# Optimization experiments

Measured on AMD Instinct MI355X. Metric: run time of the kernel, lower is better.

## Reference

```python
import jax, jax.numpy as jnp
import numpy as np

N = 50000   # nodes
E = 800000  # edges (avg degree 16)
D = 64      # node/edge feature dim
L = 3       # num_layers


def setup_inputs() -> dict:
    key = jax.random.key(0)
    ks = jax.random.split(key, 16)
    s = 0.05
    inp = {
        "x": jax.random.normal(ks[0], (N, D), jnp.float32),
        "edge_index": jax.random.randint(ks[1], (2, E), 0, N),
        "edge_attr": jax.random.normal(ks[2], (E, D), jnp.float32),
        # conv params (stacked over layers)
        "Wr": jax.random.normal(ks[3], (L, D, D), jnp.float32) * s,
        "Wn": jax.random.normal(ks[4], (L, D, D), jnp.float32) * s,
        "We": jax.random.normal(ks[5], (L, D, D), jnp.float32) * s,
        "b":  jax.random.normal(ks[6], (L, D), jnp.float32) * s,
        # EdgeMLP params (stacked over layers; only first L-1 used)
        "EWe": jax.random.normal(ks[7], (L, D, D), jnp.float32) * s,
        "Ebe": jax.random.normal(ks[8], (L, D), jnp.float32) * s,
        "EWs": jax.random.normal(ks[9], (L, D, D), jnp.float32) * s,
        "Ebs": jax.random.normal(ks[10], (L, D), jnp.float32) * s,
        "EWt": jax.random.normal(ks[11], (L, D, D), jnp.float32) * s,
        "Ebt": jax.random.normal(ks[12], (L, D), jnp.float32) * s,
        "EW1": jax.random.normal(ks[13], (L, D, D), jnp.float32) * s,
        "Eb1": jax.random.normal(ks[14], (L, D), jnp.float32) * s,
    }
    return inp


def reference(x, edge_index, edge_attr, Wr, Wn, We, b,
              EWe, Ebe, EWs, Ebs, EWt, Ebt, EW1, Eb1):
    src, dst = edge_index[0], edge_index[1]
    # in-degree for mean aggregation (static across layers)
    deg = jax.ops.segment_sum(jnp.ones((E,), x.dtype), dst, num_segments=N)
    inv_deg = (1.0 / jnp.clip(deg, 1.0))[:, None]  # [N,1]

    for i in range(L):
        # conv: message = x_src @ Wn + edge_attr @ We ; mean-aggregate at dst
        msg = x[src] @ Wn[i] + edge_attr @ We[i]              # [E,D]
        agg = jax.ops.segment_sum(msg, dst, num_segments=N) * inv_deg
        x = x @ Wr[i] + agg + b[i]                            # [N,D]
        if i == L - 1:
            break  # no act/norm/dropout/edge-update after last conv
        x = jax.nn.relu(x)  # act (norm=None, act_first=False, dropout p=0)
        # EdgeMLP: lin_e(ea) + lin_s(x)[src] + lin_t(x)[dst] -> act -> lin1
        h = (edge_attr @ EWe[i] + Ebe[i]
             + (x @ EWs[i] + Ebs[i])[src]
             + (x @ EWt[i] + Ebt[i])[dst])                    # [E,D]
        edge_attr = jax.nn.relu(h) @ EW1[i] + Eb1[i]
    return (x, edge_attr)
```

## Files before the change

### kernel.cpp

```cpp
#include <hip/hip_runtime.h>

#define D 64
#define LAYERS 3

typedef float  f4  __attribute__((ext_vector_type(4)));
typedef short  s8v __attribute__((ext_vector_type(8)));
typedef short  s4v __attribute__((ext_vector_type(4)));
typedef unsigned short ushort_t;

__device__ __forceinline__ unsigned short f2bf(float x) {
    unsigned int u = __float_as_uint(x);
    unsigned int r = (u + 0x7fffu + ((u >> 16) & 1u)) >> 16;
    return (unsigned short)r;
}
__device__ __forceinline__ float bf2f(unsigned short h) {
    return __uint_as_float(((unsigned int)h) << 16);
}


__global__ void k_count(const int* __restrict__ dst, int* __restrict__ cnt, int E) {
    int e = blockIdx.x * blockDim.x + threadIdx.x;
    if (e < E) atomicAdd(&cnt[dst[e]], 1);
}

__global__ __launch_bounds__(1024) void k_scan(const int* __restrict__ cnt,
                                               int* __restrict__ row_start,
                                               float* __restrict__ inv_deg, int N) {
    __shared__ int buf[1024];
    int tid = threadIdx.x;
    int per = (N + 1023) >> 10;
    int begin = tid * per;
    int end = min(begin + per, N);
    int s = 0;
    for (int i = begin; i < end; i++) s += cnt[i];
    buf[tid] = s;
    __syncthreads();
    for (int off = 1; off < 1024; off <<= 1) {
        int v = 0;
        if (tid >= off) v = buf[tid - off];
        __syncthreads();
        buf[tid] += v;
        __syncthreads();
    }
    int run = buf[tid] - s;
    for (int i = begin; i < end; i++) {
        row_start[i] = run;
        int c = cnt[i];
        inv_deg[i] = 1.0f / (float)(c > 1 ? c : 1);
        run += c;
    }
    if (begin < N && end == N) row_start[N] = run;
}

__global__ void k_fill(const int* __restrict__ src, const int* __restrict__ dst,
                       const int* __restrict__ row_start, int* __restrict__ cursor,
                       int* __restrict__ eids, int* __restrict__ srcs,
                       int* __restrict__ pdst, int* __restrict__ pos, int E) {
    int e = blockIdx.x * blockDim.x + threadIdx.x;
    if (e >= E) return;
    int d = dst[e];
    int p = row_start[d] + atomicAdd(&cursor[d], 1);
    eids[p] = e;
    srcs[p] = src[e];
    pdst[p] = d;
    pos[e] = p;
}

__global__ __launch_bounds__(256) void k_permcvt(const float* __restrict__ ea,
                                                 const int* __restrict__ pos,
                                                 ushort_t* __restrict__ pea, int E,
                                                 const float* __restrict__ x,
                                                 ushort_t* __restrict__ xb, int xtotal8,
                                                 int pblocks) {
    if ((int)blockIdx.x < pblocks) {
        int t = blockIdx.x * blockDim.x + threadIdx.x;
        int e = t >> 3;
        if (e >= E) return;
        int seg = t & 7;
        const float* rp = ea + (size_t)e * D + seg * 8;
        f4 a0 = *(const f4*)rp;
        f4 a1 = *(const f4*)(rp + 4);
        s8v o;
        #pragma unroll
        for (int i = 0; i < 4; i++) {
            o[i]     = (short)f2bf(a0[i]);
            o[4 + i] = (short)f2bf(a1[i]);
        }
        int p = pos[e];
        *(s8v*)(pea + (size_t)p * D + seg * 8) = o;
    } else {
        int t = (blockIdx.x - pblocks) * blockDim.x + threadIdx.x;
        if (t >= xtotal8) return;
        const float* rp = x + (size_t)t * 8;
        f4 a0 = *(const f4*)rp;
        f4 a1 = *(const f4*)(rp + 4);
        s8v o;
        #pragma unroll
        for (int i = 0; i < 4; i++) {
            o[i]     = (short)f2bf(a0[i]);
            o[4 + i] = (short)f2bf(a1[i]);
        }
        *(s8v*)(xb + (size_t)t * 8) = o;
    }
}

__global__ __launch_bounds__(64) void k_prepw(const float* __restrict__ Wr,
                                              const float* __restrict__ Wn,
                                              const float* __restrict__ Wec,
                                              const float* __restrict__ EWe,
                                              const float* __restrict__ EW1,
                                              const float* __restrict__ EWs,
                                              const float* __restrict__ EWt,
                                              s8v* __restrict__ wbuf) {
    int set = blockIdx.x;
    const float* Wsrc;
    int order, part;
    if (set < 18) {
        int i = set / 6, r = set % 6, m = r >> 1;
        part = r & 1;
        order = 0;
        const float* base = (m == 0) ? Wr : (m == 1) ? Wn : Wec;
        Wsrc = base + (size_t)i * D * D;
    } else if (set < 24) {
        int j = (set - 18) / 3, r = (set - 18) % 3;
        if (r == 2) { Wsrc = EW1 + (size_t)j * D * D; part = 2; order = 1; }
        else        { Wsrc = EWe + (size_t)j * D * D; part = r; order = 0; }
    } else {
        int j = (set - 24) / 2, r = (set - 24) % 2;
        Wsrc = ((r == 0) ? EWs : EWt) + (size_t)j * D * D;
        part = 2; order = 1;
    }
    int lane = threadIdx.x;
    int c = lane & 15, g = lane >> 4;
    s8v* wb = wbuf + (size_t)set * 512;
    #pragma unroll
    for (int nt = 0; nt < 4; nt++) {
        #pragma unroll
        for (int kt = 0; kt < 2; kt++) {
            s8v frag;
            #pragma unroll
            for (int i = 0; i < 8; i++) {
                int k = (order == 0) ? (32 * kt + 8 * g + i)
                                     : (32 * kt + 16 * (i >> 2) + 4 * g + (i & 3));
                float w = Wsrc[k * D + 16 * nt + c];
                unsigned short hb = f2bf(w);
                frag[i] = (part == 1) ? (short)f2bf(w - bf2f(hb)) : (short)hb;
            }
            wb[(nt * 2 + kt) * 64 + lane] = frag;
        }
    }
}

__global__ __launch_bounds__(256) void k_agg_seq(const ushort_t* __restrict__ xb,
                                                 const ushort_t* __restrict__ pea,
                                                 const int* __restrict__ row_start,
                                                 const int* __restrict__ srcs,
                                                 ushort_t* __restrict__ Sx, ushort_t* __restrict__ Se,
                                                 int N) {
    int n = blockIdx.x * 4 + threadIdx.y;
    if (n >= N) return;
    int j = threadIdx.x;
    int p0 = row_start[n], p1 = row_start[n + 1];
    float ax0 = 0.f, ax1 = 0.f, ax2 = 0.f, ax3 = 0.f;
    float ax4 = 0.f, ax5 = 0.f, ax6 = 0.f, ax7 = 0.f;
    float ae0 = 0.f, ae1 = 0.f, ae2 = 0.f, ae3 = 0.f;
    float ae4 = 0.f, ae5 = 0.f, ae6 = 0.f, ae7 = 0.f;
    int p = p0;
    for (; p + 8 <= p1; p += 8) {
        int s0 = srcs[p],     s1 = srcs[p + 1], s2 = srcs[p + 2], s3 = srcs[p + 3];
        int s4 = srcs[p + 4], s5 = srcs[p + 5], s6 = srcs[p + 6], s7 = srcs[p + 7];
        ax0 += bf2f(xb[(size_t)s0 * D + j]);
        ax1 += bf2f(xb[(size_t)s1 * D + j]);
        ax2 += bf2f(xb[(size_t)s2 * D + j]);
        ax3 += bf2f(xb[(size_t)s3 * D + j]);
        ax4 += bf2f(xb[(size_t)s4 * D + j]);
        ax5 += bf2f(xb[(size_t)s5 * D + j]);
        ax6 += bf2f(xb[(size_t)s6 * D + j]);
        ax7 += bf2f(xb[(size_t)s7 * D + j]);
        ae0 += bf2f(pea[(size_t)p * D + j]);
        ae1 += bf2f(pea[(size_t)(p + 1) * D + j]);
        ae2 += bf2f(pea[(size_t)(p + 2) * D + j]);
        ae3 += bf2f(pea[(size_t)(p + 3) * D + j]);
        ae4 += bf2f(pea[(size_t)(p + 4) * D + j]);
        ae5 += bf2f(pea[(size_t)(p + 5) * D + j]);
        ae6 += bf2f(pea[(size_t)(p + 6) * D + j]);
        ae7 += bf2f(pea[(size_t)(p + 7) * D + j]);
    }
    for (; p + 4 <= p1; p += 4) {
        int s0 = srcs[p], s1 = srcs[p + 1], s2 = srcs[p + 2], s3 = srcs[p + 3];
        ax0 += bf2f(xb[(size_t)s0 * D + j]);
        ax1 += bf2f(xb[(size_t)s1 * D + j]);
        ax2 += bf2f(xb[(size_t)s2 * D + j]);
        ax3 += bf2f(xb[(size_t)s3 * D + j]);
        ae0 += bf2f(pea[(size_t)p * D + j]);
        ae1 += bf2f(pea[(size_t)(p + 1) * D + j]);
        ae2 += bf2f(pea[(size_t)(p + 2) * D + j]);
        ae3 += bf2f(pea[(size_t)(p + 3) * D + j]);
    }
    for (; p < p1; p++) {
        ax0 += bf2f(xb[(size_t)srcs[p] * D + j]);
        ae0 += bf2f(pea[(size_t)p * D + j]);
    }
    float axs = ((ax0 + ax1) + (ax2 + ax3)) + ((ax4 + ax5) + (ax6 + ax7));
    float aes = ((ae0 + ae1) + (ae2 + ae3)) + ((ae4 + ae5) + (ae6 + ae7));
    Sx[(size_t)n * D + j] = f2bf(axs);
    Se[(size_t)n * D + j] = f2bf(aes);
}

template<int DO_ST, int LAST>
__global__ __launch_bounds__(256) void k_node_mfma(
        const ushort_t* __restrict__ xb_in,
        const ushort_t* __restrict__ Sx, const ushort_t* __restrict__ Se,
        const float* __restrict__ inv_deg,
        const s8v* __restrict__ wbn,
        const float* __restrict__ bias,
        const s8v* __restrict__ wbst,
        const float* __restrict__ bs, const float* __restrict__ bt,
        const float* __restrict__ be,
        float* __restrict__ xo_f32, ushort_t* __restrict__ xo_b,
        ushort_t* __restrict__ sfb, ushort_t* __restrict__ tfb, int N) {
    int lane = threadIdx.x & 63;
    int wid  = threadIdx.x >> 6;
    int c = lane & 15;
    int g = lane >> 4;

    f4 biasv[4], bsv[4], btv[4];
    #pragma unroll
    for (int nt = 0; nt < 4; nt++) {
        biasv[nt] = *(const f4*)&bias[16 * nt + 4 * g];
        if (DO_ST) {
            bsv[nt] = *(const f4*)&bs[16 * nt + 4 * g] + *(const f4*)&be[16 * nt + 4 * g];
            btv[nt] = *(const f4*)&bt[16 * nt + 4 * g];
        }
    }

    int tiles = (N + 15) >> 4;
    for (int t = blockIdx.x * 4 + wid; t < tiles; t += gridDim.x * 4) {
        int idx = t * 16 + c;
        int ic = idx < N ? idx : N - 1;
        const ushort_t* xr  = xb_in + (size_t)ic * D;
        const ushort_t* sxr = Sx + (size_t)ic * D;
        const ushort_t* ser = Se + (size_t)ic * D;
        s8v xf[2], sxf[2], sef[2];
        #pragma unroll
        for (int kt = 0; kt < 2; kt++) {
            xf[kt]  = *(const s8v*)(xr  + 32 * kt + 8 * g);
            sxf[kt] = *(const s8v*)(sxr + 32 * kt + 8 * g);
            sef[kt] = *(const s8v*)(ser + 32 * kt + 8 * g);
        }
        float inv = inv_deg[ic];

        f4 a0[4], a1[4], a2[4];
        #pragma unroll
        for (int nt = 0; nt < 4; nt++) {
            a0[nt] = (f4){0.f, 0.f, 0.f, 0.f};
            a1[nt] = (f4){0.f, 0.f, 0.f, 0.f};
            a2[nt] = (f4){0.f, 0.f, 0.f, 0.f};
        }
        #pragma unroll
        for (int nt = 0; nt < 4; nt++) {
            #pragma unroll
            for (int kt = 0; kt < 2; kt++) {
                int fo = (nt * 2 + kt) * 64 + lane;
                a0[nt] = __builtin_amdgcn_mfma_f32_16x16x32_bf16(wbn[0 * 512 + fo], xf[kt],  a0[nt], 0, 0, 0);
                a0[nt] = __builtin_amdgcn_mfma_f32_16x16x32_bf16(wbn[1 * 512 + fo], xf[kt],  a0[nt], 0, 0, 0);
                a1[nt] = __builtin_amdgcn_mfma_f32_16x16x32_bf16(wbn[2 * 512 + fo], sxf[kt], a1[nt], 0, 0, 0);
                a1[nt] = __builtin_amdgcn_mfma_f32_16x16x32_bf16(wbn[3 * 512 + fo], sxf[kt], a1[nt], 0, 0, 0);
                a2[nt] = __builtin_amdgcn_mfma_f32_16x16x32_bf16(wbn[4 * 512 + fo], sef[kt], a2[nt], 0, 0, 0);
                a2[nt] = __builtin_amdgcn_mfma_f32_16x16x32_bf16(wbn[5 * 512 + fo], sef[kt], a2[nt], 0, 0, 0);
            }
        }

        f4 v[4];
        #pragma unroll
        for (int nt = 0; nt < 4; nt++) {
            #pragma unroll
            for (int r = 0; r < 4; r++) {
                float vv = a0[nt][r] + inv * (a1[nt][r] + a2[nt][r]) + biasv[nt][r];
                v[nt][r] = LAST ? vv : fmaxf(vv, 0.f);
            }
        }

        if (idx < N) {
            if (LAST) {
                float* orow = xo_f32 + (size_t)idx * D;
                #pragma unroll
                for (int nt = 0; nt < 4; nt++) *(f4*)&orow[16 * nt + 4 * g] = v[nt];
            } else {
                ushort_t* orow = xo_b + (size_t)idx * D;
                #pragma unroll
                for (int nt = 0; nt < 4; nt++) {
                    s4v ov;
                    #pragma unroll
                    for (int r = 0; r < 4; r++) ov[r] = (short)f2bf(v[nt][r]);
                    *(s4v*)(orow + 16 * nt + 4 * g) = ov;
                }
            }
        }

        if (DO_ST) {
            s8v hf[2];
            #pragma unroll
            for (int nt = 0; nt < 4; nt++) {
                #pragma unroll
                for (int r = 0; r < 4; r++) {
                    hf[nt >> 1][((nt & 1) << 2) + r] = (short)f2bf(v[nt][r]);
                }
            }
            f4 so[4], to[4];
            #pragma unroll
            for (int nt = 0; nt < 4; nt++) {
                so[nt] = (f4){0.f, 0.f, 0.f, 0.f};
                to[nt] = (f4){0.f, 0.f, 0.f, 0.f};
            }
            #pragma unroll
            for (int nt = 0; nt < 4; nt++) {
                #pragma unroll
                for (int kt = 0; kt < 2; kt++) {
                    int fo = (nt * 2 + kt) * 64 + lane;
                    so[nt] = __builtin_amdgcn_mfma_f32_16x16x32_bf16(wbst[0 * 512 + fo], hf[kt], so[nt], 0, 0, 0);
                    to[nt] = __builtin_amdgcn_mfma_f32_16x16x32_bf16(wbst[1 * 512 + fo], hf[kt], to[nt], 0, 0, 0);
                }
            }
            if (idx < N) {
                ushort_t* srow = sfb + (size_t)idx * D;
                ushort_t* trow = tfb + (size_t)idx * D;
                #pragma unroll
                for (int nt = 0; nt < 4; nt++) {
                    s4v sv, tv;
                    #pragma unroll
                    for (int r = 0; r < 4; r++) {
                        sv[r] = (short)f2bf(so[nt][r] + bsv[nt][r]);
                        tv[r] = (short)f2bf(to[nt][r] + btv[nt][r]);
                    }
                    *(s4v*)(srow + 16 * nt + 4 * g) = sv;
                    *(s4v*)(trow + 16 * nt + 4 * g) = tv;
                }
            }
        }
    }
}

template<int MODE>
__global__ __launch_bounds__(256, 2) void k_edge_mfma(
        const ushort_t* ea_in,
        const int* __restrict__ srcA, const int* __restrict__ dstA,
        const int* __restrict__ emap,
        const ushort_t* __restrict__ sfb, const ushort_t* __restrict__ tfb,
        const s8v* __restrict__ wb,
        const float* __restrict__ b1,
        ushort_t* out_p, float* __restrict__ out_e, int E) {
    int lane = threadIdx.x & 63;
    int wid  = threadIdx.x >> 6;
    int c = lane & 15;
    int g = lane >> 4;

    s8v weh[4][2], wel[4][2], w1f[4][2];
    #pragma unroll
    for (int nt = 0; nt < 4; nt++) {
        #pragma unroll
        for (int kt = 0; kt < 2; kt++) {
            int f = nt * 2 + kt;
            weh[nt][kt] = wb[0 * 512 + f * 64 + lane];
            wel[nt][kt] = wb[1 * 512 + f * 64 + lane];
            w1f[nt][kt] = wb[2 * 512 + f * 64 + lane];
        }
    }
    f4 b1v[4];
    #pragma unroll
    for (int nt = 0; nt < 4; nt++) {
        b1v[nt] = *(const f4*)&b1[16 * nt + 4 * g];
    }

    int tiles = (E + 15) >> 4;
    int S = gridDim.x * 4;
    int t = blockIdx.x * 4 + wid;
    if (t >= tiles) return;

    int idx = t * 16 + c;
    int ic = idx < E ? idx : E - 1;
    const ushort_t* ear = ea_in + (size_t)ic * D;
    s8v ea0v = *(const s8v*)(ear + 8 * g);
    s8v ea1v = *(const s8v*)(ear + 32 + 8 * g);
    int s  = srcA[ic];
    int d2 = dstA[ic];
    int em = (MODE == 1) ? emap[ic] : 0;

    while (true) {
        int tn = t + S;
        bool more = (tn < tiles);
        int idxn = more ? tn * 16 + c : idx;
        int icn = idxn < E ? idxn : E - 1;
        const ushort_t* earn = ea_in + (size_t)icn * D;
        s8v ean0 = *(const s8v*)(earn + 8 * g);
        s8v ean1 = *(const s8v*)(earn + 32 + 8 * g);
        int sn  = srcA[icn];
        int dn  = dstA[icn];
        int emn = (MODE == 1) ? emap[icn] : 0;

        const ushort_t* sr = sfb + (size_t)s * D;
        const ushort_t* tr = tfb + (size_t)d2 * D;
        s4v sgv[4], tgv[4];
        #pragma unroll
        for (int nt = 0; nt < 4; nt++) {
            sgv[nt] = *(const s4v*)(sr + 16 * nt + 4 * g);
            tgv[nt] = *(const s4v*)(tr + 16 * nt + 4 * g);
        }

        f4 acc[4];
        #pragma unroll
        for (int nt = 0; nt < 4; nt++) acc[nt] = (f4){0.f, 0.f, 0.f, 0.f};
        #pragma unroll
        for (int nt = 0; nt < 4; nt++) {
            #pragma unroll
            for (int kt = 0; kt < 2; kt++) {
                s8v av = (kt == 0) ? ea0v : ea1v;
                acc[nt] = __builtin_amdgcn_mfma_f32_16x16x32_bf16(weh[nt][kt], av, acc[nt], 0, 0, 0);
                acc[nt] = __builtin_amdgcn_mfma_f32_16x16x32_bf16(wel[nt][kt], av, acc[nt], 0, 0, 0);
            }
        }

        s8v hf[2];
        #pragma unroll
        for (int nt = 0; nt < 4; nt++) {
            #pragma unroll
            for (int r = 0; r < 4; r++) {
                float hv = acc[nt][r] + bf2f((ushort_t)sgv[nt][r]) + bf2f((ushort_t)tgv[nt][r]);
                hv = fmaxf(hv, 0.f);
                hf[nt >> 1][((nt & 1) << 2) + r] = (short)f2bf(hv);
            }
        }

        f4 out[4];
        #pragma unroll
        for (int nt = 0; nt < 4; nt++) out[nt] = (f4){0.f, 0.f, 0.f, 0.f};
        #pragma unroll
        for (int nt = 0; nt < 4; nt++) {
            #pragma unroll
            for (int kt = 0; kt < 2; kt++) {
                out[nt] = __builtin_amdgcn_mfma_f32_16x16x32_bf16(w1f[nt][kt], hf[kt], out[nt], 0, 0, 0);
            }
        }

        if (idx < E) {
            #pragma unroll
            for (int nt = 0; nt < 4; nt++) out[nt] += b1v[nt];
            ushort_t* prow = out_p + (size_t)idx * D;
            #pragma unroll
            for (int nt = 0; nt < 4; nt++) {
                s4v ov;
                #pragma unroll
                for (int r = 0; r < 4; r++) ov[r] = (short)f2bf(out[nt][r]);
                *(s4v*)(prow + 16 * nt + 4 * g) = ov;
            }
            if (MODE == 1) {
                float* orow = out_e + (size_t)em * D;
                #pragma unroll
                for (int nt = 0; nt < 4; nt++) *(f4*)&orow[16 * nt + 4 * g] = out[nt];
            }
        }

        if (!more) break;
        t = tn; idx = idxn;
        ea0v = ean0; ea1v = ean1; s = sn; d2 = dn; em = emn;
    }
}

extern "C" void kernel_launch(void* const* d_in, const int* in_sizes, int n_in,
                              void* d_out, int out_size, void* d_ws, size_t ws_size,
                              hipStream_t stream) {
    const float* x0  = (const float*)d_in[0];
    const int*   ei  = (const int*)d_in[1];
    const float* ea0 = (const float*)d_in[2];
    const float* Wr  = (const float*)d_in[3];
    const float* Wn  = (const float*)d_in[4];
    const float* We  = (const float*)d_in[5];
    const float* b   = (const float*)d_in[6];
    const float* EWe = (const float*)d_in[7];
    const float* Ebe = (const float*)d_in[8];
    const float* EWs = (const float*)d_in[9];
    const float* Ebs = (const float*)d_in[10];
    const float* EWt = (const float*)d_in[11];
    const float* Ebt = (const float*)d_in[12];
    const float* EW1 = (const float*)d_in[13];
    const float* Eb1 = (const float*)d_in[14];

    const int N = in_sizes[0] / D;
    const int E = in_sizes[1] / 2;
    const int* src = ei;
    const int* dst = ei + E;

    char* ws = (char*)d_ws;
    size_t off = 0;
    auto alloc = [&](size_t bytes) {
        void* p = ws + off;
        off += (bytes + 255) & ~(size_t)255;
        return p;
    };
    int*      cntcur    = (int*)alloc((size_t)2 * N * 4);
    int*      cnt       = cntcur;
    int*      cursor    = cntcur + N;
    int*      row_start = (int*)alloc((size_t)(N + 1) * 4);
    int*      eids      = (int*)alloc((size_t)E * 4);
    int*      srcs      = (int*)alloc((size_t)E * 4);
    int*      pdst      = (int*)alloc((size_t)E * 4);
    int*      pos       = (int*)alloc((size_t)E * 4);
    float*    inv_deg   = (float*)alloc((size_t)N * 4);
    ushort_t* Sx        = (ushort_t*)alloc((size_t)N * D * 2);
    ushort_t* Se        = (ushort_t*)alloc((size_t)N * D * 2);
    ushort_t* xb0       = (ushort_t*)alloc((size_t)N * D * 2);
    ushort_t* xb1       = (ushort_t*)alloc((size_t)N * D * 2);
    ushort_t* sfb       = (ushort_t*)alloc((size_t)N * D * 2);
    ushort_t* tfb       = (ushort_t*)alloc((size_t)N * D * 2);
    s8v*      wbuf      = (s8v*)alloc((size_t)28 * 512 * 16);
    ushort_t* pea       = (ushort_t*)alloc((size_t)E * D * 2);

    float* outx  = (float*)d_out;
    float* outea = (float*)d_out + (size_t)N * D;

    hipMemsetAsync(cntcur, 0, (size_t)2 * N * 4, stream);
    k_count<<<(E + 255) / 256, 256, 0, stream>>>(dst, cnt, E);
    k_scan<<<1, 1024, 0, stream>>>(cnt, row_start, inv_deg, N);
    k_fill<<<(E + 255) / 256, 256, 0, stream>>>(src, dst, row_start, cursor, eids, srcs, pdst, pos, E);
    {
        int pblocks = (E * 8 + 255) / 256;
        int xblocks = (N * D / 8 + 255) / 256;
        k_permcvt<<<pblocks + xblocks, 256, 0, stream>>>(ea0, pos, pea, E, x0, xb0, N * D / 8, pblocks);
    }
    k_prepw<<<28, 64, 0, stream>>>(Wr, Wn, We, EWe, EW1, EWs, EWt, wbuf);

    dim3 b644(64, 4);
    const s8v* wbn0  = wbuf;
    const s8v* wbn1  = wbuf + 6 * 512;
    const s8v* wbn2  = wbuf + 12 * 512;
    const s8v* wbe0  = wbuf + 18 * 512;
    const s8v* wbe1  = wbuf + 21 * 512;
    const s8v* wbst0 = wbuf + 24 * 512;
    const s8v* wbst1 = wbuf + 26 * 512;

    k_agg_seq<<<(N + 3) / 4, b644, 0, stream>>>(xb0, pea, row_start, srcs, Sx, Se, N);
    k_node_mfma<1, 0><<<1024, 256, 0, stream>>>(xb0, Sx, Se, inv_deg, wbn0, b,
                                                wbst0, Ebs, Ebt, Ebe,
                                                nullptr, xb1, sfb, tfb, N);
    k_edge_mfma<0><<<2048, 256, 0, stream>>>(pea, srcs, pdst, eids, sfb, tfb,
                                             wbe0, Eb1, pea, nullptr, E);

    k_agg_seq<<<(N + 3) / 4, b644, 0, stream>>>(xb1, pea, row_start, srcs, Sx, Se, N);
    k_node_mfma<1, 0><<<1024, 256, 0, stream>>>(xb1, Sx, Se, inv_deg, wbn1, b + D,
                                                wbst1, Ebs + D, Ebt + D, Ebe + D,
                                                nullptr, xb0, sfb, tfb, N);
    k_edge_mfma<1><<<2048, 256, 0, stream>>>(pea, srcs, pdst, eids, sfb, tfb,
                                             wbe1, Eb1 + D, pea, outea, E);

    k_agg_seq<<<(N + 3) / 4, b644, 0, stream>>>(xb0, pea, row_start, srcs, Sx, Se, N);
    k_node_mfma<0, 1><<<1024, 256, 0, stream>>>(xb0, Sx, Se, inv_deg, wbn2, b + 2 * D,
                                                nullptr, nullptr, nullptr, nullptr,
                                                outx, nullptr, nullptr, nullptr, N);
}
```

Measured before the change: 653.4 us.

## Fuse edge-attr permute into fill and vectorize neighbor aggregation across edges

The edge-attribute bf16 conversion and CSR permutation now happen inside k_fill, one thread per edge writing a whole 64-wide row. This removes the pos array and the separate permute pass, and x conversion gets its own small kernel. The aggregation kernel now has each wavefront process 8 edges at once, each lane loading 16-byte vectors, and combines the partial sums with xor shuffles. This replaces the per-feature scalar 2-byte loads. The cost is less coalesced per-thread reads in k_fill and shuffle-reduction overhead for low-degree nodes.

Result: no change. 659.7 us (+1.0%).

```diff
diff --git a/kernel.cpp b/kernel.cpp
--- a/kernel.cpp
+++ b/kernel.cpp
@@ -55,7 +55,8 @@
 __global__ void k_fill(const int* __restrict__ src, const int* __restrict__ dst,
                        const int* __restrict__ row_start, int* __restrict__ cursor,
                        int* __restrict__ eids, int* __restrict__ srcs,
-                       int* __restrict__ pdst, int* __restrict__ pos, int E) {
+                       int* __restrict__ pdst,
+                       const float* __restrict__ ea, ushort_t* __restrict__ pea, int E) {
     int e = blockIdx.x * blockDim.x + threadIdx.x;
     if (e >= E) return;
     int d = dst[e];
@@ -63,45 +64,36 @@
     eids[p] = e;
     srcs[p] = src[e];
     pdst[p] = d;
-    pos[e] = p;
-}
-
-__global__ __launch_bounds__(256) void k_permcvt(const float* __restrict__ ea,
-                                                 const int* __restrict__ pos,
-                                                 ushort_t* __restrict__ pea, int E,
-                                                 const float* __restrict__ x,
-                                                 ushort_t* __restrict__ xb, int xtotal8,
-                                                 int pblocks) {
-    if ((int)blockIdx.x < pblocks) {
-        int t = blockIdx.x * blockDim.x + threadIdx.x;
-        int e = t >> 3;
-        if (e >= E) return;
-        int seg = t & 7;
-        const float* rp = ea + (size_t)e * D + seg * 8;
-        f4 a0 = *(const f4*)rp;
-        f4 a1 = *(const f4*)(rp + 4);
+    const float* rp = ea + (size_t)e * D;
+    ushort_t* wp = pea + (size_t)p * D;
+    #pragma unroll
+    for (int seg = 0; seg < 8; seg++) {
+        f4 a0 = *(const f4*)(rp + seg * 8);
+        f4 a1 = *(const f4*)(rp + seg * 8 + 4);
         s8v o;
         #pragma unroll
         for (int i = 0; i < 4; i++) {
             o[i]     = (short)f2bf(a0[i]);
             o[4 + i] = (short)f2bf(a1[i]);
         }
-        int p = pos[e];
-        *(s8v*)(pea + (size_t)p * D + seg * 8) = o;
-    } else {
-        int t = (blockIdx.x - pblocks) * blockDim.x + threadIdx.x;
-        if (t >= xtotal8) return;
-        const float* rp = x + (size_t)t * 8;
-        f4 a0 = *(const f4*)rp;
-        f4 a1 = *(const f4*)(rp + 4);
-        s8v o;
-        #pragma unroll
-        for (int i = 0; i < 4; i++) {
-            o[i]     = (short)f2bf(a0[i]);
-            o[4 + i] = (short)f2bf(a1[i]);
-        }
-        *(s8v*)(xb + (size_t)t * 8) = o;
-    }
+        *(s8v*)(wp + seg * 8) = o;
+    }
+}
+
+__global__ __launch_bounds__(256) void k_xcvt(const float* __restrict__ x,
+                                              ushort_t* __restrict__ xb, int total8) {
+    int t = blockIdx.x * blockDim.x + threadIdx.x;
+    if (t >= total8) return;
+    const float* rp = x + (size_t)t * 8;
+    f4 a0 = *(const f4*)rp;
+    f4 a1 = *(const f4*)(rp + 4);
+    s8v o;
+    #pragma unroll
+    for (int i = 0; i < 4; i++) {
+        o[i]     = (short)f2bf(a0[i]);
+        o[4 + i] = (short)f2bf(a1[i]);
+    }
+    *(s8v*)(xb + (size_t)t * 8) = o;
 }
 
 __global__ __launch_bounds__(64) void k_prepw(const float* __restrict__ Wr,
@@ -159,52 +151,46 @@
                                                  int N) {
     int n = blockIdx.x * 4 + threadIdx.y;
     if (n >= N) return;
-    int j = threadIdx.x;
+    int lane = threadIdx.x;
+    int r = lane >> 3;
+    int o = lane & 7;
     int p0 = row_start[n], p1 = row_start[n + 1];
-    float ax0 = 0.f, ax1 = 0.f, ax2 = 0.f, ax3 = 0.f;
-    float ax4 = 0.f, ax5 = 0.f, ax6 = 0.f, ax7 = 0.f;
-    float ae0 = 0.f, ae1 = 0.f, ae2 = 0.f, ae3 = 0.f;
-    float ae4 = 0.f, ae5 = 0.f, ae6 = 0.f, ae7 = 0.f;
-    int p = p0;
-    for (; p + 8 <= p1; p += 8) {
-        int s0 = srcs[p],     s1 = srcs[p + 1], s2 = srcs[p + 2], s3 = srcs[p + 3];
-        int s4 = srcs[p + 4], s5 = srcs[p + 5], s6 = srcs[p + 6], s7 = srcs[p + 7];
-        ax0 += bf2f(xb[(size_t)s0 * D + j]);
-        ax1 += bf2f(xb[(size_t)s1 * D + j]);
-        ax2 += bf2f(xb[(size_t)s2 * D + j]);
-        ax3 += bf2f(xb[(size_t)s3 * D + j]);
-        ax4 += bf2f(xb[(size_t)s4 * D + j]);
-        ax5 += bf2f(xb[(size_t)s5 * D + j]);
-        ax6 += bf2f(xb[(size_t)s6 * D + j]);
-        ax7 += bf2f(xb[(size_t)s7 * D + j]);
-        ae0 += bf2f(pea[(size_t)p * D + j]);
-        ae1 += bf2f(pea[(size_t)(p + 1) * D + j]);
-        ae2 += bf2f(pea[(size_t)(p + 2) * D + j]);
-        ae3 += bf2f(pea[(size_t)(p + 3) * D + j]);
-        ae4 += bf2f(pea[(size_t)(p + 4) * D + j]);
-        ae5 += bf2f(pea[(size_t)(p + 5) * D + j]);
-        ae6 += bf2f(pea[(size_t)(p + 6) * D + j]);
-        ae7 += bf2f(pea[(size_t)(p + 7) * D + j]);
-    }
-    for (; p + 4 <= p1; p += 4) {
-        int s0 = srcs[p], s1 = srcs[p + 1], s2 = srcs[p + 2], s3 = srcs[p + 3];
-        ax0 += bf2f(xb[(size_t)s0 * D + j]);
-        ax1 += bf2f(xb[(size_t)s1 * D + j]);
-        ax2 += bf2f(xb[(size_t)s2 * D + j]);
-        ax3 += bf2f(xb[(size_t)s3 * D + j]);
-        ae0 += bf2f(pea[(size_t)p * D + j]);
-        ae1 += bf2f(pea[(size_t)(p + 1) * D + j]);
-        ae2 += bf2f(pea[(size_t)(p + 2) * D + j]);
-        ae3 += bf2f(pea[(size_t)(p + 3) * D + j]);
-    }
-    for (; p < p1; p++) {
-        ax0 += bf2f(xb[(size_t)srcs[p] * D + j]);
-        ae0 += bf2f(pea[(size_t)p * D + j]);
-    }
-    float axs = ((ax0 + ax1) + (ax2 + ax3)) + ((ax4 + ax5) + (ax6 + ax7));
-    float aes = ((ae0 + ae1) + (ae2 + ae3)) + ((ae4 + ae5) + (ae6 + ae7));
-    Sx[(size_t)n * D + j] = f2bf(axs);
-    Se[(size_t)n * D + j] = f2bf(aes);
+    f4 ax0 = (f4){0.f, 0.f, 0.f, 0.f}, ax1 = (f4){0.f, 0.f, 0.f, 0.f};
+    f4 ae0 = (f4){0.f, 0.f, 0.f, 0.f}, ae1 = (f4){0.f, 0.f, 0.f, 0.f};
+    for (int p = p0 + r; p < p1; p += 8) {
+        s8v ev = *(const s8v*)(pea + (size_t)p * D + o * 8);
+        int sidx = srcs[p];
+        s8v xv = *(const s8v*)(xb + (size_t)sidx * D + o * 8);
+        #pragma unroll
+        for (int i = 0; i < 4; i++) {
+            ae0[i] += bf2f((ushort_t)ev[i]);
+            ae1[i] += bf2f((ushort_t)ev[4 + i]);
+            ax0[i] += bf2f((ushort_t)xv[i]);
+            ax1[i] += bf2f((ushort_t)xv[4 + i]);
+        }
+    }
+    #pragma unroll
+    for (int off = 8; off < 64; off <<= 1) {
+        #pragma unroll
+        for (int i = 0; i < 4; i++) {
+            ax0[i] += __shfl_xor(ax0[i], off);
+            ax1[i] += __shfl_xor(ax1[i], off);
+            ae0[i] += __shfl_xor(ae0[i], off);
+            ae1[i] += __shfl_xor(ae1[i], off);
+        }
+    }
+    if (r == 0) {
+        s8v sx, se;
+        #pragma unroll
+        for (int i = 0; i < 4; i++) {
+            sx[i]     = (short)f2bf(ax0[i]);
+            sx[4 + i] = (short)f2bf(ax1[i]);
+            se[i]     = (short)f2bf(ae0[i]);
+            se[4 + i] = (short)f2bf(ae1[i]);
+        }
+        *(s8v*)(Sx + (size_t)n * D + o * 8) = sx;
+        *(s8v*)(Se + (size_t)n * D + o * 8) = se;
+    }
 }
 
 template<int DO_ST, int LAST>
@@ -504,7 +490,6 @@
     int*      eids      = (int*)alloc((size_t)E * 4);
     int*      srcs      = (int*)alloc((size_t)E * 4);
     int*      pdst      = (int*)alloc((size_t)E * 4);
-    int*      pos       = (int*)alloc((size_t)E * 4);
     float*    inv_deg   = (float*)alloc((size_t)N * 4);
     ushort_t* Sx        = (ushort_t*)alloc((size_t)N * D * 2);
     ushort_t* Se        = (ushort_t*)alloc((size_t)N * D * 2);
@@ -521,12 +506,9 @@
     hipMemsetAsync(cntcur, 0, (size_t)2 * N * 4, stream);
     k_count<<<(E + 255) / 256, 256, 0, stream>>>(dst, cnt, E);
     k_scan<<<1, 1024, 0, stream>>>(cnt, row_start, inv_deg, N);
-    k_fill<<<(E + 255) / 256, 256, 0, stream>>>(src, dst, row_start, cursor, eids, srcs, pdst, pos, E);
-    {
-        int pblocks = (E * 8 + 255) / 256;
-        int xblocks = (N * D / 8 + 255) / 256;
-        k_permcvt<<<pblocks + xblocks, 256, 0, stream>>>(ea0, pos, pea, E, x0, xb0, N * D / 8, pblocks);
-    }
+    k_fill<<<(E + 255) / 256, 256, 0, stream>>>(src, dst, row_start, cursor,
+                                                eids, srcs, pdst, ea0, pea, E);
+    k_xcvt<<<(N * D / 8 + 255) / 256, 256, 0, stream>>>(x0, xb0, N * D / 8);
     k_prepw<<<28, 64, 0, stream>>>(Wr, Wn, We, EWe, EW1, EWs, EWt, wbuf);
 
     dim3 b644(64, 4);
```
